# Kernel tuning notes

Hardware: AMD Instinct MI355X
Metric: run time of the kernel (lower is better)

## Reference

```python
import jax, jax.numpy as jnp
import numpy as np

B, S, DIM, H = 2, 2048, 1536, 12
HD = DIM // H  # 128
EPS = 1e-6


def setup_inputs() -> dict:
    key = jax.random.key(0)
    ks = jax.random.split(key, 6)
    x = jax.random.normal(ks[0], (B, S, DIM), dtype=jnp.float32)
    # RoPE rotation as (cos, sin) pairs: shape [S, 1, HD//2, 2]
    inv = 1.0 / (10000.0 ** (np.arange(0, HD, 2, dtype=np.float32) / HD))
    ang = np.arange(S, dtype=np.float32)[:, None] * inv[None, :]  # [S, HD//2]
    freqs = jnp.asarray(np.stack([np.cos(ang), np.sin(ang)], axis=-1))[:, None, :, :]
    def lin(k):
        return jax.random.normal(k, (DIM, DIM), dtype=jnp.float32) * 0.02
    wq, wk, wv, wo = lin(ks[1]), lin(ks[2]), lin(ks[3]), lin(ks[4])
    zb = jnp.zeros((DIM,), dtype=jnp.float32)
    ones = jnp.ones((DIM,), dtype=jnp.float32)
    return dict(x=x, freqs=freqs,
                wq=wq, bq=zb, wk=wk, bk=zb, wv=wv, bv=zb, wo=wo, bo=zb,
                gq=ones, gk=ones, timestep=500)


def reference(x, freqs, wq, bq, wk, bk, wv, bv, wo, bo, gq, gk, timestep):
    b, s, dim = x.shape

    def rms(z, g):
        zf = z.astype(jnp.float32)
        n = zf * jax.lax.rsqrt(jnp.mean(zf * zf, axis=-1, keepdims=True) + EPS)
        return n.astype(z.dtype) * g

    def rope(t):
        # [b,s,dim] -> [b,s,H,HD//2,2] pairs; complex multiply by freqs
        tp = t.reshape(b, s, H, HD // 2, 2)
        tr, ti = tp[..., 0], tp[..., 1]
        fr = freqs[None, ..., 0]  # [1,s,1,HD//2] broadcasts over batch & heads
        fi = freqs[None, ..., 1]
        out = jnp.stack([tr * fr - ti * fi, tr * fi + ti * fr], axis=-1)
        return out.reshape(b, s, dim)

    q = rope(rms(x @ wq.T + bq, gq))
    k = rope(rms(x @ wk.T + bk, gk))
    v = x @ wv.T + bv

    qh = q.reshape(b, s, H, HD).transpose(0, 2, 1, 3)
    kh = k.reshape(b, s, H, HD).transpose(0, 2, 1, 3)
    vh = v.reshape(b, s, H, HD).transpose(0, 2, 1, 3)
    scores = jnp.einsum('bhqd,bhkd->bhqk', qh, kh) / np.float32(np.sqrt(HD))
    attn = jax.nn.softmax(scores, axis=-1)
    out = jnp.einsum('bhqk,bhkd->bhqd', attn, vh)
    out = out.transpose(0, 2, 1, 3).reshape(b, s, dim)
    return out @ wo.T + bo
```

## Files before the change

### kernel.cpp

```cpp
#include <hip/hip_runtime.h>
#include <hip/hip_bf16.h>


#define BQ  2
#define SQ  2048
#define DIMQ 1536
#define HQ  12
#define HDQ 128
#define MTOK 4096
#define KDIM 1536

typedef __attribute__((ext_vector_type(8))) short short8;
typedef __attribute__((ext_vector_type(4))) float f32x4;
typedef __attribute__((ext_vector_type(16))) float f32x16;
typedef __attribute__((ext_vector_type(8))) unsigned short u16x8;

typedef __attribute__((address_space(1))) const void global_cvoid;
typedef __attribute__((address_space(3))) void lds_void;

__device__ __forceinline__ float bf2f(unsigned int u) {
    return __uint_as_float(u << 16);
}
__device__ __forceinline__ unsigned short f2bf(float f) {
    unsigned int u = __float_as_uint(f);
    u += 0x7fffu + ((u >> 16) & 1u);
    return (unsigned short)(u >> 16);
}
__device__ __forceinline__ void gload_lds16(const void* g, void* l) {
    __builtin_amdgcn_global_load_lds((global_cvoid*)g, (lds_void*)l, 16, 0, 0);
}
__device__ __forceinline__ unsigned int cvtpk_bf16(float lo, float hi) {
    unsigned int r;
    asm("v_cvt_pk_bf16_f32 %0, %1, %2" : "=v"(r) : "v"(lo), "v"(hi));
    return r;
}

#define VMCNT(n) asm volatile("s_waitcnt vmcnt(" #n ")" ::: "memory")
#define MEMFENCE() asm volatile("" ::: "memory")
#define BARRIER() do { asm volatile("" ::: "memory"); \
                       __builtin_amdgcn_s_barrier();  \
                       asm volatile("" ::: "memory"); } while (0)

__global__ __launch_bounds__(256)
void cast_all(const float* __restrict__ x,
              const float* __restrict__ wq, const float* __restrict__ wk,
              const float* __restrict__ wv, const float* __restrict__ wo,
              unsigned short* __restrict__ Xb,
              unsigned short* __restrict__ Wqkv,
              unsigned short* __restrict__ Wob)
{
    const int NX = 1572864, NW = 589824;
    int i = blockIdx.x * blockDim.x + threadIdx.x;
    int stride = gridDim.x * blockDim.x;
    for (; i < NX + 4 * NW; i += stride) {
        const float* s; unsigned short* d; int off;
        if (i < NX) { s = x; d = Xb; off = i; }
        else {
            int j = i - NX;
            int seg = j / NW;
            off = j - seg * NW;
            s = (seg == 0) ? wq : (seg == 1) ? wk : (seg == 2) ? wv : wo;
            d = (seg < 3) ? (Wqkv + seg * 2359296) : Wob;
        }
        float4 v = ((const float4*)s)[off];
        unsigned short a = f2bf(v.x), b = f2bf(v.y), c = f2bf(v.z), e = f2bf(v.w);
        unsigned int lo = (unsigned int)a | ((unsigned int)b << 16);
        unsigned int hi = (unsigned int)c | ((unsigned int)e << 16);
        ((uint2*)d)[off] = make_uint2(lo, hi);
    }
}

template<int MODE>
__global__ __launch_bounds__(256)
void gemm_bt(const unsigned short* __restrict__ A,
             const unsigned short* __restrict__ Bm,
             unsigned short* __restrict__ oQ,
             unsigned short* __restrict__ oK,
             unsigned short* __restrict__ oV,
             const float* __restrict__ biasq,
             const float* __restrict__ biask,
             const float* __restrict__ biasv,
             float* __restrict__ oF,
             const float* __restrict__ biaso)
{
    __shared__ unsigned short ldsA[2][128 * 32];
    __shared__ unsigned short ldsB[2][128 * 32];
    const int m0 = blockIdx.x * 128;
    const int n0 = blockIdx.y * 128;
    const int t = threadIdx.x;
    const int lane = t & 63;
    const int wid = t >> 6;
    const int wr = (wid >> 1) * 64;
    const int wc = (wid & 1) * 64;
    const int lr = lane & 15;
    const int lk = lane >> 4;

    f32x4 acc[4][4] = {};

    #pragma unroll
    for (int i = 0; i < 2; ++i) {
        const int off = i * 4096 + wid * 1024 + lane * 16;
        const int r = off >> 6;
        const int c = (off >> 4) & 3;
        const int csw = (c ^ (r & 3)) << 3;
        gload_lds16(A + (size_t)(m0 + r) * KDIM + csw,
                    (char*)ldsA[0] + i * 4096 + wid * 1024);
        gload_lds16(Bm + (size_t)(n0 + r) * KDIM + csw,
                    (char*)ldsB[0] + i * 4096 + wid * 1024);
    }

    #pragma unroll 1
    for (int s = 0; s < KDIM / 32; ++s) {
        const int cb = s & 1;
        if (s + 1 < KDIM / 32) {
            const int kt = (s + 1) * 32;
            #pragma unroll
            for (int i = 0; i < 2; ++i) {
                const int off = i * 4096 + wid * 1024 + lane * 16;
                const int r = off >> 6;
                const int c = (off >> 4) & 3;
                const int csw = (c ^ (r & 3)) << 3;
                gload_lds16(A + (size_t)(m0 + r) * KDIM + kt + csw,
                            (char*)ldsA[cb ^ 1] + i * 4096 + wid * 1024);
                gload_lds16(Bm + (size_t)(n0 + r) * KDIM + kt + csw,
                            (char*)ldsB[cb ^ 1] + i * 4096 + wid * 1024);
            }
            VMCNT(4);
        } else {
            VMCNT(0);
        }
        BARRIER();

        short8 af[4], bf[4];
        #pragma unroll
        for (int mi = 0; mi < 4; ++mi) {
            int row = wr + mi * 16 + lr;
            int ch = lk ^ (row & 3);
            af[mi] = *(const short8*)((const char*)ldsA[cb] + row * 64 + ch * 16);
        }
        #pragma unroll
        for (int ni = 0; ni < 4; ++ni) {
            int row = wc + ni * 16 + lr;
            int ch = lk ^ (row & 3);
            bf[ni] = *(const short8*)((const char*)ldsB[cb] + row * 64 + ch * 16);
        }
        #pragma unroll
        for (int mi = 0; mi < 4; ++mi)
            #pragma unroll
            for (int ni = 0; ni < 4; ++ni)
                acc[mi][ni] = __builtin_amdgcn_mfma_f32_16x16x32_bf16(
                    af[mi], bf[ni], acc[mi][ni], 0, 0, 0);

        BARRIER();
    }

    if (MODE == 0) {
        const int seg = n0 / 1536;
        unsigned short* op = (seg == 0) ? oQ : (seg == 1 ? oK : oV);
        const float* bp = (seg == 0) ? biasq : (seg == 1 ? biask : biasv);
        const int nl0 = n0 - seg * 1536;
        #pragma unroll
        for (int mi = 0; mi < 4; ++mi)
            #pragma unroll
            for (int ni = 0; ni < 4; ++ni)
                #pragma unroll
                for (int j = 0; j < 4; ++j) {
                    int row = m0 + wr + mi * 16 + lk * 4 + j;
                    int col = nl0 + wc + ni * 16 + lr;
                    op[(size_t)row * 1536 + col] = f2bf(acc[mi][ni][j] + bp[col]);
                }
    } else {
        #pragma unroll
        for (int mi = 0; mi < 4; ++mi)
            #pragma unroll
            for (int ni = 0; ni < 4; ++ni)
                #pragma unroll
                for (int j = 0; j < 4; ++j) {
                    int row = m0 + wr + mi * 16 + lk * 4 + j;
                    int col = n0 + wc + ni * 16 + lr;
                    oF[(size_t)row * 1536 + col] = acc[mi][ni][j] + biaso[col];
                }
    }
}

__global__ __launch_bounds__(256)
void rmsnorm_rope(unsigned short* __restrict__ Qb,
                  unsigned short* __restrict__ Kb,
                  const float* __restrict__ gq,
                  const float* __restrict__ gk,
                  const float* __restrict__ freqs)
{
    unsigned short* T = blockIdx.y ? Kb : Qb;
    const float* g = blockIdx.y ? gk : gq;
    const int token = blockIdx.x;
    const int s = token & (SQ - 1);
    unsigned int* row = (unsigned int*)(T + (size_t)token * DIMQ);
    const int t = threadIdx.x;
    const int lane = t & 63, wid = t >> 6;

    float pr[3], pi[3];
    float ss = 0.f;
    #pragma unroll
    for (int q = 0; q < 3; ++q) {
        unsigned int v = row[t + q * 256];
        float a = bf2f(v & 0xffffu);
        float b = bf2f(v >> 16);
        pr[q] = a; pi[q] = b;
        ss += a * a + b * b;
    }
    ss += __shfl_xor(ss, 32); ss += __shfl_xor(ss, 16); ss += __shfl_xor(ss, 8);
    ss += __shfl_xor(ss, 4);  ss += __shfl_xor(ss, 2);  ss += __shfl_xor(ss, 1);
    __shared__ float red[4];
    if (lane == 0) red[wid] = ss;
    __syncthreads();
    float tot = red[0] + red[1] + red[2] + red[3];
    float sc = rsqrtf(tot * (1.0f / 1536.0f) + 1e-6f);

    #pragma unroll
    for (int q = 0; q < 3; ++q) {
        int p = t + q * 256;
        int ph = p & 63;
        float fr = freqs[s * 128 + ph * 2];
        float fi = freqs[s * 128 + ph * 2 + 1];
        float nr = pr[q] * sc * g[2 * p];
        float ni = pi[q] * sc * g[2 * p + 1];
        float outr = nr * fr - ni * fi;
        float outi = nr * fi + ni * fr;
        row[p] = (unsigned int)f2bf(outr) | ((unsigned int)f2bf(outi) << 16);
    }
}

__global__ __launch_bounds__(256)
void vtrans(const unsigned short* __restrict__ V, unsigned short* __restrict__ Vt)
{
    __shared__ unsigned short tile[64][72];
    const int s0 = blockIdx.x * 64;
    const int d0 = blockIdx.y * 64;
    const int bh = blockIdx.z;
    const int b = bh / HQ, h = bh % HQ;
    const int t = threadIdx.x;

    #pragma unroll
    for (int i = 0; i < 2; ++i) {
        int cid = i * 256 + t;
        int r = cid >> 3, c = cid & 7;
        u16x8 v = *(const u16x8*)(V + (size_t)(b * SQ + s0 + r) * DIMQ + h * HDQ + d0 + c * 8);
        #pragma unroll
        for (int e = 0; e < 8; ++e) tile[r][c * 8 + e] = v[e];
    }
    __syncthreads();
    #pragma unroll
    for (int i = 0; i < 2; ++i) {
        int cid = i * 256 + t;
        int rd = cid >> 3, c = cid & 7;
        u16x8 w;
        #pragma unroll
        for (int e = 0; e < 8; ++e) w[e] = tile[c * 8 + e][rd];
        *(u16x8*)(Vt + (size_t)(bh * HDQ + d0 + rd) * SQ + s0 + c * 8) = w;
    }
}

__global__ __launch_bounds__(64, 2)
void attn(const unsigned short* __restrict__ Q,
          const unsigned short* __restrict__ Kb,
          const unsigned short* __restrict__ Vt,
          unsigned short* __restrict__ Ao)
{
    __shared__ char smem[24576];
    char* Kl0 = smem;
    char* Kl1 = smem + 8192;
    char* Vl  = smem + 16384;

    const int fid = blockIdx.x;
    const int xcd = fid & 7;
    const int slot = fid >> 3;
    const int bh = xcd * 3 + (slot >> 6);
    const int sblk = slot & 63;
    const int b = bh / HQ, h = bh % HQ;
    const int s0 = sblk * 32;

    const int lane = threadIdx.x;
    const int l31 = lane & 31, hi = lane >> 5;
    const float CE = 0.12751879f;
    const float THR = 90.5f;

    const unsigned short* Kbase = Kb + (size_t)(b * SQ) * DIMQ + h * HDQ;
    const unsigned short* Vbase = Vt + (size_t)(bh * HDQ) * SQ;

    short8 qf[8];
    {
        const unsigned short* qp = Q + (size_t)(b * SQ + s0 + l31) * DIMQ + h * HDQ;
        #pragma unroll
        for (int kc = 0; kc < 8; ++kc)
            qf[kc] = *(const short8*)(qp + kc * 16 + hi * 8);
    }
    MEMFENCE();
    #pragma unroll
    for (int i = 0; i < 8; ++i) {
        const int off = i * 1024 + lane * 16;
        int r = off >> 8, c = (off >> 4) & 15;
        gload_lds16(Kbase + (size_t)r * DIMQ + ((c ^ (r & 7)) << 3), Kl0 + i * 1024);
    }
    VMCNT(8);

    char* kcur = Kl0;
    char* knxt = Kl1;
    float mrun = -1e30f, lsum = 0.f, nm = 1e30f;
    f32x16 oacc[4] = {};

    #pragma unroll 1
    for (int kv0 = 0; kv0 < SQ; kv0 += 32) {
        #pragma unroll
        for (int i = 0; i < 8; ++i) {
            const int off = i * 1024 + lane * 16;
            int r = off >> 6, c = (off >> 4) & 3;
            gload_lds16(Vbase + (size_t)r * SQ + kv0 + ((c ^ ((r >> 1) & 3)) << 3),
                        Vl + i * 1024);
        }
        MEMFENCE();
        const int kvn = (kv0 + 32 < SQ) ? kv0 + 32 : kv0;
        #pragma unroll
        for (int i = 0; i < 8; ++i) {
            const int off = i * 1024 + lane * 16;
            int r = off >> 8, c = (off >> 4) & 15;
            gload_lds16(Kbase + (size_t)(kvn + r) * DIMQ + ((c ^ (r & 7)) << 3),
                        knxt + i * 1024);
        }

        VMCNT(16);

        f32x16 sa = {}, sb = {};
        const int rb = l31 * 256;
        const int rx = l31 & 7;
        #pragma unroll
        for (int kc = 0; kc < 4; ++kc) {
            short8 kf = *(const short8*)(kcur + rb + (((kc * 2 + hi) ^ rx) << 4));
            sa = __builtin_amdgcn_mfma_f32_32x32x16_bf16(kf, qf[kc], sa, 0, 0, 0);
        }
        #pragma unroll
        for (int kc = 4; kc < 8; ++kc) {
            short8 kf = *(const short8*)(kcur + rb + (((kc * 2 + hi) ^ rx) << 4));
            sb = __builtin_amdgcn_mfma_f32_32x32x16_bf16(kf, qf[kc], sb, 0, 0, 0);
        }
        f32x16 s;
        #pragma unroll
        for (int r = 0; r < 16; ++r) s[r] = sa[r] + sb[r];

        float mt[8];
        #pragma unroll
        for (int r = 0; r < 8; ++r) mt[r] = fmaxf(s[r], s[r + 8]);
        #pragma unroll
        for (int st = 4; st > 0; st >>= 1)
            #pragma unroll
            for (int r = 0; r < 4; ++r)
                if (r < st) mt[r] = fmaxf(mt[r], mt[r + st]);
        float tm = fmaxf(mt[0], __shfl_xor(mt[0], 32));
        if (!__all(tm <= mrun + THR)) {
            float mnew = fmaxf(mrun, tm);
            float al = __builtin_amdgcn_exp2f((mrun - mnew) * CE);
            lsum *= al;
            #pragma unroll
            for (int dt = 0; dt < 4; ++dt)
                #pragma unroll
                for (int r = 0; r < 16; ++r) oacc[dt][r] *= al;
            mrun = mnew;
            nm = -mrun * CE;
        }
        float rs = 0.f;
        #pragma unroll
        for (int r = 0; r < 16; ++r) {
            float p = __builtin_amdgcn_exp2f(__builtin_fmaf(s[r], CE, nm));
            s[r] = p; rs += p;
        }
        rs += __shfl_xor(rs, 32);
        lsum += rs;

        unsigned int A0 = cvtpk_bf16(s[0], s[1]),  A1 = cvtpk_bf16(s[2], s[3]);
        unsigned int B0 = cvtpk_bf16(s[4], s[5]),  B1 = cvtpk_bf16(s[6], s[7]);
        unsigned int C0 = cvtpk_bf16(s[8], s[9]),  C1 = cvtpk_bf16(s[10], s[11]);
        unsigned int D0 = cvtpk_bf16(s[12], s[13]), D1 = cvtpk_bf16(s[14], s[15]);
        unsigned int xA0 = __shfl_xor(A0, 32), xA1 = __shfl_xor(A1, 32);
        unsigned int xB0 = __shfl_xor(B0, 32), xB1 = __shfl_xor(B1, 32);
        unsigned int xC0 = __shfl_xor(C0, 32), xC1 = __shfl_xor(C1, 32);
        unsigned int xD0 = __shfl_xor(D0, 32), xD1 = __shfl_xor(D1, 32);
        union { unsigned int w[4]; short8 v; } pf0, pf1;
        pf0.w[0] = hi ? xB0 : A0;  pf0.w[1] = hi ? xB1 : A1;
        pf0.w[2] = hi ? B0 : xA0;  pf0.w[3] = hi ? B1 : xA1;
        pf1.w[0] = hi ? xD0 : C0;  pf1.w[1] = hi ? xD1 : C1;
        pf1.w[2] = hi ? D0 : xC0;  pf1.w[3] = hi ? D1 : xC1;

        VMCNT(8);

        #pragma unroll
        for (int dt = 0; dt < 4; ++dt) {
            const int drow = dt * 32 + l31;
            const int sw = (drow >> 1) & 3;
            short8 v0 = *(const short8*)(Vl + drow * 64 + ((hi ^ sw) << 4));
            short8 v1 = *(const short8*)(Vl + drow * 64 + (((2 + hi) ^ sw) << 4));
            oacc[dt] = __builtin_amdgcn_mfma_f32_32x32x16_bf16(v0, pf0.v, oacc[dt], 0, 0, 0);
            oacc[dt] = __builtin_amdgcn_mfma_f32_32x32x16_bf16(v1, pf1.v, oacc[dt], 0, 0, 0);
        }

        char* tp = kcur; kcur = knxt; knxt = tp;
    }

    const float rls = 1.0f / lsum;
    char* Ot = Vl;
    #pragma unroll
    for (int dt = 0; dt < 4; ++dt)
        #pragma unroll
        for (int rp = 0; rp < 8; ++rp) {
            const int r = 2 * rp;
            float v0 = oacc[dt][r] * rls;
            float v1 = oacc[dt][r + 1] * rls;
            int d = dt * 32 + (r & 3) + 8 * (r >> 2) + 4 * hi;
            unsigned int w = (unsigned int)f2bf(v0) | ((unsigned int)f2bf(v1) << 16);
            int addr = l31 * 256 + (((d >> 3) ^ (l31 & 7)) << 4) + (d & 7) * 2;
            *(unsigned int*)(Ot + addr) = w;
        }
    #pragma unroll
    for (int ii = 0; ii < 8; ++ii) {
        int task = ii * 64 + lane;
        int q = task >> 4, c = task & 15;
        u16x8 vv = *(const u16x8*)(Ot + q * 256 + ((c ^ (q & 7)) << 4));
        int tok = b * SQ + s0 + q;
        *(u16x8*)(Ao + (size_t)tok * DIMQ + h * HDQ + c * 8) = vv;
    }
}

extern "C" void kernel_launch(void* const* d_in, const int* in_sizes, int n_in,
                              void* d_out, int out_size, void* d_ws, size_t ws_size,
                              hipStream_t stream) {
    (void)in_sizes; (void)n_in; (void)out_size; (void)ws_size;
    const float* x     = (const float*)d_in[0];
    const float* freqs = (const float*)d_in[1];
    const float* wq = (const float*)d_in[2];
    const float* bq = (const float*)d_in[3];
    const float* wk = (const float*)d_in[4];
    const float* bk = (const float*)d_in[5];
    const float* wv = (const float*)d_in[6];
    const float* bv = (const float*)d_in[7];
    const float* wo = (const float*)d_in[8];
    const float* bo = (const float*)d_in[9];
    const float* gq = (const float*)d_in[10];
    const float* gk = (const float*)d_in[11];
    float* out = (float*)d_out;

    char* w = (char*)d_ws;
    unsigned short* Xb   = (unsigned short*)(w);
    unsigned short* Wqkv = (unsigned short*)(w + 12582912);
    unsigned short* Wob  = (unsigned short*)(w + 26738688);
    unsigned short* Qb   = (unsigned short*)(w + 31457280);
    unsigned short* Kbuf = (unsigned short*)(w + 44040192);
    unsigned short* Vb   = (unsigned short*)(w + 56623104);
    unsigned short* Vt   = (unsigned short*)(w + 69206016);
    unsigned short* Ao   = Xb;

    cast_all<<<2048, 256, 0, stream>>>(x, wq, wk, wv, wo, Xb, Wqkv, Wob);

    gemm_bt<0><<<dim3(32, 36), 256, 0, stream>>>(
        Xb, Wqkv, Qb, Kbuf, Vb, bq, bk, bv, nullptr, nullptr);

    rmsnorm_rope<<<dim3(4096, 2), 256, 0, stream>>>(Qb, Kbuf, gq, gk, freqs);
    vtrans<<<dim3(32, 2, 24), 256, 0, stream>>>(Vb, Vt);

    attn<<<1536, 64, 0, stream>>>(Qb, Kbuf, Vt, Ao);

    gemm_bt<1><<<dim3(32, 12), 256, 0, stream>>>(
        Ao, Wob, nullptr, nullptr, nullptr, nullptr, nullptr, nullptr, out, bo);
}
```

Before: 245.6 us.

## Fuse V transpose into QKV GEMM epilogue via shared-memory staging

The QKV GEMM epilogue for V tiles now stages the bf16 output in a swizzled shared-memory tile and writes it out transposed straight into the Vt layout ([b*h, d, s]). This removes the separate vtrans kernel launch and its extra global read and write of V. The LDS arrays are merged into one 32KB buffer that is reused for staging, which adds a barrier and LDS traffic to the epilogue of the V blocks only.

```diff
diff --git a/kernel.cpp b/kernel.cpp
--- a/kernel.cpp
+++ b/kernel.cpp
@@ -83,8 +83,7 @@
              float* __restrict__ oF,
              const float* __restrict__ biaso)
 {
-    __shared__ unsigned short ldsA[2][128 * 32];
-    __shared__ unsigned short ldsB[2][128 * 32];
+    __shared__ char smem[32768];
     const int m0 = blockIdx.x * 128;
     const int n0 = blockIdx.y * 128;
     const int t = threadIdx.x;
@@ -104,9 +103,9 @@
         const int c = (off >> 4) & 3;
         const int csw = (c ^ (r & 3)) << 3;
         gload_lds16(A + (size_t)(m0 + r) * KDIM + csw,
-                    (char*)ldsA[0] + i * 4096 + wid * 1024);
+                    smem + i * 4096 + wid * 1024);
         gload_lds16(Bm + (size_t)(n0 + r) * KDIM + csw,
-                    (char*)ldsB[0] + i * 4096 + wid * 1024);
+                    smem + 16384 + i * 4096 + wid * 1024);
     }
 
     #pragma unroll 1
@@ -121,9 +120,9 @@
                 const int c = (off >> 4) & 3;
                 const int csw = (c ^ (r & 3)) << 3;
                 gload_lds16(A + (size_t)(m0 + r) * KDIM + kt + csw,
-                            (char*)ldsA[cb ^ 1] + i * 4096 + wid * 1024);
+                            smem + (cb ^ 1) * 8192 + i * 4096 + wid * 1024);
                 gload_lds16(Bm + (size_t)(n0 + r) * KDIM + kt + csw,
-                            (char*)ldsB[cb ^ 1] + i * 4096 + wid * 1024);
+                            smem + 16384 + (cb ^ 1) * 8192 + i * 4096 + wid * 1024);
             }
             VMCNT(4);
         } else {
@@ -136,13 +135,13 @@
         for (int mi = 0; mi < 4; ++mi) {
             int row = wr + mi * 16 + lr;
             int ch = lk ^ (row & 3);
-            af[mi] = *(const short8*)((const char*)ldsA[cb] + row * 64 + ch * 16);
+            af[mi] = *(const short8*)(smem + cb * 8192 + row * 64 + ch * 16);
         }
         #pragma unroll
         for (int ni = 0; ni < 4; ++ni) {
             int row = wc + ni * 16 + lr;
             int ch = lk ^ (row & 3);
-            bf[ni] = *(const short8*)((const char*)ldsB[cb] + row * 64 + ch * 16);
+            bf[ni] = *(const short8*)(smem + 16384 + cb * 8192 + row * 64 + ch * 16);
         }
         #pragma unroll
         for (int mi = 0; mi < 4; ++mi)
@@ -156,19 +155,46 @@
 
     if (MODE == 0) {
         const int seg = n0 / 1536;
-        unsigned short* op = (seg == 0) ? oQ : (seg == 1 ? oK : oV);
-        const float* bp = (seg == 0) ? biasq : (seg == 1 ? biask : biasv);
         const int nl0 = n0 - seg * 1536;
-        #pragma unroll
-        for (int mi = 0; mi < 4; ++mi)
-            #pragma unroll
-            for (int ni = 0; ni < 4; ++ni)
+        if (seg < 2) {
+            unsigned short* op = (seg == 0) ? oQ : oK;
+            const float* bp = (seg == 0) ? biasq : biask;
+            #pragma unroll
+            for (int mi = 0; mi < 4; ++mi)
                 #pragma unroll
-                for (int j = 0; j < 4; ++j) {
-                    int row = m0 + wr + mi * 16 + lk * 4 + j;
-                    int col = nl0 + wc + ni * 16 + lr;
-                    op[(size_t)row * 1536 + col] = f2bf(acc[mi][ni][j] + bp[col]);
-                }
+                for (int ni = 0; ni < 4; ++ni)
+                    #pragma unroll
+                    for (int j = 0; j < 4; ++j) {
+                        int row = m0 + wr + mi * 16 + lk * 4 + j;
+                        int col = nl0 + wc + ni * 16 + lr;
+                        op[(size_t)row * 1536 + col] = f2bf(acc[mi][ni][j] + bp[col]);
+                    }
+        } else {
+            #pragma unroll
+            for (int mi = 0; mi < 4; ++mi)
+                #pragma unroll
+                for (int ni = 0; ni < 4; ++ni)
+                    #pragma unroll
+                    for (int j = 0; j < 4; ++j) {
+                        int sl = wr + mi * 16 + lk * 4 + j;
+                        int dl = wc + ni * 16 + lr;
+                        unsigned short val = f2bf(acc[mi][ni][j] + biasv[nl0 + dl]);
+                        *(unsigned short*)(smem + dl * 256 +
+                            ((((sl >> 3) ^ (dl & 15))) << 4) + (sl & 7) * 2) = val;
+                    }
+            BARRIER();
+            const int h = nl0 >> 7;
+            const int bb = m0 >> 11;
+            const int sseq0 = m0 & 2047;
+            const int bh = bb * HQ + h;
+            #pragma unroll
+            for (int p = 0; p < 8; ++p) {
+                int d = wid * 32 + p * 4 + lk;
+                int sc = lr;
+                u16x8 v = *(const u16x8*)(smem + d * 256 + ((sc ^ (d & 15)) << 4));
+                *(u16x8*)(oV + (size_t)(bh * HDQ + d) * SQ + sseq0 + sc * 8) = v;
+            }
+        }
     } else {
         #pragma unroll
         for (int mi = 0; mi < 4; ++mi)
@@ -227,36 +253,6 @@
         float outr = nr * fr - ni * fi;
         float outi = nr * fi + ni * fr;
         row[p] = (unsigned int)f2bf(outr) | ((unsigned int)f2bf(outi) << 16);
-    }
-}
-
-__global__ __launch_bounds__(256)
-void vtrans(const unsigned short* __restrict__ V, unsigned short* __restrict__ Vt)
-{
-    __shared__ unsigned short tile[64][72];
-    const int s0 = blockIdx.x * 64;
-    const int d0 = blockIdx.y * 64;
-    const int bh = blockIdx.z;
-    const int b = bh / HQ, h = bh % HQ;
-    const int t = threadIdx.x;
-
-    #pragma unroll
-    for (int i = 0; i < 2; ++i) {
-        int cid = i * 256 + t;
-        int r = cid >> 3, c = cid & 7;
-        u16x8 v = *(const u16x8*)(V + (size_t)(b * SQ + s0 + r) * DIMQ + h * HDQ + d0 + c * 8);
-        #pragma unroll
-        for (int e = 0; e < 8; ++e) tile[r][c * 8 + e] = v[e];
-    }
-    __syncthreads();
-    #pragma unroll
-    for (int i = 0; i < 2; ++i) {
-        int cid = i * 256 + t;
-        int rd = cid >> 3, c = cid & 7;
-        u16x8 w;
-        #pragma unroll
-        for (int e = 0; e < 8; ++e) w[e] = tile[c * 8 + e][rd];
-        *(u16x8*)(Vt + (size_t)(bh * HDQ + d0 + rd) * SQ + s0 + c * 8) = w;
     }
 }
 
@@ -452,17 +448,15 @@
     unsigned short* Wob  = (unsigned short*)(w + 26738688);
     unsigned short* Qb   = (unsigned short*)(w + 31457280);
     unsigned short* Kbuf = (unsigned short*)(w + 44040192);
-    unsigned short* Vb   = (unsigned short*)(w + 56623104);
     unsigned short* Vt   = (unsigned short*)(w + 69206016);
     unsigned short* Ao   = Xb;
 
     cast_all<<<2048, 256, 0, stream>>>(x, wq, wk, wv, wo, Xb, Wqkv, Wob);
 
     gemm_bt<0><<<dim3(32, 36), 256, 0, stream>>>(
-        Xb, Wqkv, Qb, Kbuf, Vb, bq, bk, bv, nullptr, nullptr);
+        Xb, Wqkv, Qb, Kbuf, Vt, bq, bk, bv, nullptr, nullptr);
 
     rmsnorm_rope<<<dim3(4096, 2), 256, 0, stream>>>(Qb, Kbuf, gq, gk, freqs);
-    vtrans<<<dim3(32, 2, 24), 256, 0, stream>>>(Vb, Vt);
 
     attn<<<1536, 64, 0, stream>>>(Qb, Kbuf, Vt, Ao);
 
```

Measured after the change: 236.1 us, median of 2. -3.9%, faster.
